# Optimization experiments

Hardware: AMD Instinct MI355X
Metric: run time of the kernel (lower is better)

Reference implementation:

```python
import jax, jax.numpy as jnp
import numpy as np

N_PANO, N_FP = 50000, 10000
D_IN, D_FP, HID, OUT = 128, 64, 128, 64
E_PP, E_PF = 800000, 50000


def _gat(x_src, x_dst, src, dst, Ws, Wd, a_s, a_d, b, n_dst):
    # PyG GATConv (heads=1, add_self_loops=False, bipartite lin_src/lin_dst)
    hs = x_src @ Ws                      # [Ns, C]
    hd = x_dst @ Wd                      # [Nd, C]
    es = hs @ a_s                        # [Ns]
    ed = hd @ a_d                        # [Nd]
    e = jax.nn.leaky_relu(es[src] + ed[dst], negative_slope=0.2)  # [E]
    m = jax.ops.segment_max(e, dst, num_segments=n_dst)
    ex = jnp.exp(e - m[dst])
    den = jax.ops.segment_sum(ex, dst, num_segments=n_dst)
    alpha = ex / den[dst]                # segment softmax over incoming edges
    out = jax.ops.segment_sum(hs[src] * alpha[:, None], dst, num_segments=n_dst)
    return out + b


def setup_inputs() -> dict:
    key = jax.random.key(0)
    ks = jax.random.split(key, 32)
    s_in = 1.0 / np.sqrt(D_IN)
    s_hid = 1.0 / np.sqrt(HID)
    s_fp = 1.0 / np.sqrt(D_FP)
    inp = {
        "x_pano": jax.random.normal(ks[0], (N_PANO, D_IN), jnp.float32),
        "x_fp": jax.random.normal(ks[1], (N_FP, D_FP), jnp.float32),
        # layer 0 (in = D_IN)
        "Ws0": jax.random.normal(ks[2], (D_IN, HID)) * s_in,
        "Wd0": jax.random.normal(ks[3], (D_IN, HID)) * s_in,
        "as0": jax.random.normal(ks[4], (HID,)) * 0.1,
        "ad0": jax.random.normal(ks[5], (HID,)) * 0.1,
        "b0": jnp.zeros((HID,), jnp.float32),
        "Lw0": jax.random.normal(ks[6], (D_IN, HID)) * s_in,
        "Lb0": jnp.zeros((HID,), jnp.float32),
        # layer 1 (in = HID)
        "Ws1": jax.random.normal(ks[7], (HID, HID)) * s_hid,
        "Wd1": jax.random.normal(ks[8], (HID, HID)) * s_hid,
        "as1": jax.random.normal(ks[9], (HID,)) * 0.1,
        "ad1": jax.random.normal(ks[10], (HID,)) * 0.1,
        "b1": jnp.zeros((HID,), jnp.float32),
        "Lw1": jax.random.normal(ks[11], (HID, HID)) * s_hid,
        "Lb1": jnp.zeros((HID,), jnp.float32),
        # translate conv pano -> footprint
        "Wts": jax.random.normal(ks[12], (HID, OUT)) * s_hid,
        "Wtd": jax.random.normal(ks[13], (D_FP, OUT)) * s_fp,
        "ats": jax.random.normal(ks[14], (OUT,)) * 0.1,
        "atd": jax.random.normal(ks[15], (OUT,)) * 0.1,
        "bt": jnp.zeros((OUT,), jnp.float32),
        "edge_pp": jax.random.randint(ks[16], (2, E_PP), 0, N_PANO),
        "edge_pf_src": jax.random.randint(ks[17], (E_PF,), 0, N_PANO),
        "edge_pf_dst": jax.random.randint(ks[18], (E_PF,), 0, N_FP),
    }
    return inp


def reference(x_pano, x_fp, Ws0, Wd0, as0, ad0, b0, Lw0, Lb0,
              Ws1, Wd1, as1, ad1, b1, Lw1, Lb1,
              Wts, Wtd, ats, atd, bt,
              edge_pp, edge_pf_src, edge_pf_dst):
    src, dst = edge_pp[0], edge_pp[1]
    layer_params = [(Ws0, Wd0, as0, ad0, b0, Lw0, Lb0),
                    (Ws1, Wd1, as1, ad1, b1, Lw1, Lb1)]
    h = x_pano
    for (Ws, Wd, a_s, a_d, b, Lw, Lb) in layer_params:
        conv = _gat(h, h, src, dst, Ws, Wd, a_s, a_d, b, N_PANO)
        h = jax.nn.relu(conv + h @ Lw + Lb)
    # HeteroConv with single relation + aggr='sum' == the bipartite conv output
    out_fp = _gat(h, x_fp, edge_pf_src, edge_pf_dst, Wts, Wtd, ats, atd, bt, N_FP)
    return out_fp
```

## Files before the change

kernel.cpp:

```cpp
#include <hip/hip_runtime.h>
#include <hip/hip_bf16.h>
#include <math.h>

#define N_PANO 50000
#define N_FP   10000
#define N_UNI  60000
#define HID    128
#define OUT_C  64
#define E_PP   800000
#define E_PF   50000
#define E_UNI  850000
#define NBKT   235
#define EPB    4096
#define NT_CNT 208

typedef unsigned short ushort_t;
typedef unsigned int uint_t;
typedef __attribute__((ext_vector_type(8))) short short8;
typedef __attribute__((ext_vector_type(4))) float f32x4;

static inline int cdiv(int a, int b) { return (a + b - 1) / b; }

__device__ inline ushort_t f2bf(float x) {
    __hip_bfloat16 h = __float2bfloat16(x);
    return *reinterpret_cast<ushort_t*>(&h);
}
__device__ inline float bfu2f(ushort_t u) {
    return __uint_as_float(((uint_t)u) << 16);
}
__device__ inline float bflo(uint_t u) { return __uint_as_float((u & 0xffffu) << 16); }
__device__ inline float bfhi(uint_t u) { return __uint_as_float(u & 0xffff0000u); }
__device__ inline f32x4 mfma16(short8 a, short8 b, f32x4 c) {
    return __builtin_amdgcn_mfma_f32_16x16x32_bf16(a, b, c, 0, 0, 0);
}

__global__ __launch_bounds__(256) void csr_count_prep(
        const int* __restrict__ pp_dst, const int* __restrict__ pf_dst,
        int* __restrict__ pcnt,
        const float* __restrict__ Ws0, const float* __restrict__ Lw0,
        const float* __restrict__ Ws1, const float* __restrict__ Lw1,
        const float* __restrict__ Wts,
        const float* __restrict__ Wd0, const float* __restrict__ ad0,
        const float* __restrict__ Wd1, const float* __restrict__ ad1,
        const float* __restrict__ Wtd, const float* __restrict__ atd,
        ushort_t* s0, ushort_t* l0, ushort_t* s1, ushort_t* l1, ushort_t* ts,
        float* wed0, float* wed1, float* wedt) {
    __shared__ int hist[NBKT];
    const int tile = blockIdx.x, tid = threadIdx.x;
    if (tile < NT_CNT) {
        for (int t = tid; t < NBKT; t += 256) hist[t] = 0;
        __syncthreads();
        const int e0 = tile * EPB;
        #pragma unroll
        for (int u = 0; u < 16; ++u) {
            int e = e0 + u * 256 + tid;
            int d = -1;
            if (e < E_PP) d = pp_dst[e];
            else if (e < E_UNI) d = N_PANO + pf_dst[e - E_PP];
            if (d >= 0) atomicAdd(&hist[d >> 8], 1);
        }
        __syncthreads();
        for (int t = tid; t < NBKT; t += 256) pcnt[t * NT_CNT + tile] = hist[t];
    } else if (tile < NT_CNT + 288) {
        int i = (tile - NT_CNT) * 256 + tid;
        const float* W; ushort_t* oh;
        int d, NIc, Cc;
        if (i < 65536) {
            int m = i >> 14; d = i & 16383;
            W = (m == 0) ? Ws0 : (m == 1) ? Lw0 : (m == 2) ? Ws1 : Lw1;
            oh = (m == 0) ? s0 : (m == 1) ? l0 : (m == 2) ? s1 : l1;
            NIc = 8; Cc = 128;
        } else if (i < 73728) {
            d = i - 65536; W = Wts; oh = ts;
            NIc = 4; Cc = 64;
        } else return;
        int j = d & 7, l = (d >> 3) & 63;
        int kcl = (d >> 9) & 1;
        int ni = (d >> 10) & (NIc - 1);
        int p = d >> (10 + (NIc == 8 ? 3 : 2));
        int kc = p * 2 + kcl;
        int n = ni * 16 + (l & 15);
        int k = kc * 32 + (l >> 4) * 8 + j;
        oh[d] = f2bf(W[k * Cc + n]);
    } else {
        int r = (tile - NT_CNT - 288) * 4 + (tid >> 6);
        int lane = tid & 63;
        const float* W; const float* a; float* o; int rr, C;
        if (r < 128)      { W = Wd0; a = ad0; o = wed0; rr = r;       C = 128; }
        else if (r < 256) { W = Wd1; a = ad1; o = wed1; rr = r - 128; C = 128; }
        else if (r < 320) { W = Wtd; a = atd; o = wedt; rr = r - 256; C = 64;  }
        else return;
        float s = 0.f;
        for (int j = lane; j < C; j += 64) s += W[rr * C + j] * a[j];
        #pragma unroll
        for (int off = 32; off; off >>= 1) s += __shfl_down(s, off, 64);
        if (lane == 0) o[rr] = s;
    }
}

__global__ __launch_bounds__(256) void csr_scan(const int* __restrict__ pcnt,
                                                int* __restrict__ pexc, int* __restrict__ btot) {
    __shared__ int wsum[4];
    const int b = blockIdx.x, tid = threadIdx.x, lane = tid & 63, wv = tid >> 6;
    int v = (tid < NT_CNT) ? pcnt[b * NT_CNT + tid] : 0;
    int incl = v;
    #pragma unroll
    for (int off = 1; off < 64; off <<= 1) {
        int t = __shfl_up(incl, off, 64);
        if (lane >= off) incl += t;
    }
    if (lane == 63) wsum[wv] = incl;
    __syncthreads();
    if (tid == 0) {
        int run = 0;
        #pragma unroll
        for (int w = 0; w < 4; ++w) { int t = wsum[w]; wsum[w] = run; run += t; }
    }
    __syncthreads();
    int excl = wsum[wv] + incl - v;
    if (tid < NT_CNT) pexc[b * NT_CNT + tid] = excl;
    if (tid == 255) btot[b] = excl;
}

__global__ __launch_bounds__(256) void csr_scatter(const int* __restrict__ pp_src,
                                                   const int* __restrict__ pp_dst,
                                                   const int* __restrict__ pf_src,
                                                   const int* __restrict__ pf_dst,
                                                   const int* __restrict__ pexc,
                                                   const int* __restrict__ btot,
                                                   int* __restrict__ bbase_out,
                                                   int2* __restrict__ tmp) {
    __shared__ int base2[NBKT];
    __shared__ int cur[NBKT];
    __shared__ int wsum[4];
    const int tile = blockIdx.x, tid = threadIdx.x, lane = tid & 63, wv = tid >> 6;
    int v = (tid < NBKT) ? btot[tid] : 0;
    int incl = v;
    #pragma unroll
    for (int off = 1; off < 64; off <<= 1) {
        int t = __shfl_up(incl, off, 64);
        if (lane >= off) incl += t;
    }
    if (lane == 63) wsum[wv] = incl;
    __syncthreads();
    if (tid == 0) {
        int run = 0;
        #pragma unroll
        for (int w = 0; w < 4; ++w) { int t = wsum[w]; wsum[w] = run; run += t; }
    }
    __syncthreads();
    int excl = wsum[wv] + incl - v;
    if (tid < NBKT) {
        base2[tid] = excl + pexc[tid * NT_CNT + tile];
        cur[tid] = 0;
        if (tile == 0) bbase_out[tid] = excl;
    }
    if (tile == 0 && tid == 0) bbase_out[NBKT] = E_UNI;
    __syncthreads();
    const int e0 = tile * EPB;
    #pragma unroll
    for (int u = 0; u < 16; ++u) {
        int e = e0 + u * 256 + tid;
        int d = -1, s = 0;
        if (e < E_PP)       { d = pp_dst[e];                 s = pp_src[e]; }
        else if (e < E_UNI) { d = N_PANO + pf_dst[e - E_PP]; s = pf_src[e - E_PP]; }
        if (d >= 0) {
            int b = d >> 8;
            int p = base2[b] + atomicAdd(&cur[b], 1);
            tmp[p] = make_int2(s, d);
        }
    }
}

__global__ __launch_bounds__(256) void csr_sort(const int2* __restrict__ tmp,
                                                const int* __restrict__ bbase,
                                                int* __restrict__ ptr, int* __restrict__ col) {
    __shared__ int hist[256];
    __shared__ int wsum[4];
    const int b = blockIdx.x, tid = threadIdx.x, lane = tid & 63, wv = tid >> 6;
    const int B0 = bbase[b], B1 = bbase[b + 1];
    hist[tid] = 0;
    __syncthreads();
    for (int e = B0 + tid; e < B1; e += 256) atomicAdd(&hist[tmp[e].y & 255], 1);
    __syncthreads();
    int v = hist[tid];
    int incl = v;
    #pragma unroll
    for (int off = 1; off < 64; off <<= 1) {
        int t = __shfl_up(incl, off, 64);
        if (lane >= off) incl += t;
    }
    if (lane == 63) wsum[wv] = incl;
    __syncthreads();
    if (tid == 0) {
        int run = 0;
        #pragma unroll
        for (int w = 0; w < 4; ++w) { int t = wsum[w]; wsum[w] = run; run += t; }
    }
    __syncthreads();
    int excl = wsum[wv] + incl - v;
    int dg = b * 256 + tid;
    if (dg < N_UNI) ptr[dg] = B0 + excl;
    if (b == NBKT - 1 && tid == 0) ptr[N_UNI] = E_UNI;
    hist[tid] = excl;
    __syncthreads();
    for (int e = B0 + tid; e < B1; e += 256) {
        int2 ed2 = tmp[e];
        int p = B0 + atomicAdd(&hist[ed2.y & 255], 1);
        col[p] = ed2.x;
    }
}

template <int CN, bool DUAL, bool FP32IN>
__global__ __launch_bounds__(256, 2) void gemm_mfma(const float* __restrict__ Xf,
                                                 const ushort_t* __restrict__ Xh,
                                                 const ushort_t* __restrict__ W1, const ushort_t* __restrict__ W2,
                                                 ushort_t* __restrict__ Y1, ushort_t* __restrict__ Y2,
                                                 const float* __restrict__ avec, float* __restrict__ evec,
                                                 const float* __restrict__ wed, float* __restrict__ edv,
                                                 int N) {
    constexpr int NI = CN / 16;
    constexpr int NMAT = DUAL ? 2 : 1;
    constexpr int SLAB = NI * 1024;
    __shared__ ushort_t Bsh[NMAT * SLAB];
    const int tid = threadIdx.x;
    const int w = tid >> 6, l = tid & 63;
    const int col = l & 15, q = l >> 4;
    const int row0 = blockIdx.x * 128 + w * 32;
    f32x4 acc1[2][NI];
    f32x4 acc2[2][DUAL ? NI : 1];
    #pragma unroll
    for (int m = 0; m < 2; ++m)
        #pragma unroll
        for (int ni = 0; ni < NI; ++ni)
            #pragma unroll
            for (int r = 0; r < 4; ++r) acc1[m][ni][r] = 0.f;
    if (DUAL) {
        #pragma unroll
        for (int m = 0; m < 2; ++m)
            #pragma unroll
            for (int ni = 0; ni < NI; ++ni)
                #pragma unroll
                for (int r = 0; r < 4; ++r) acc2[m][ni][r] = 0.f;
    }
    float ped[2] = {0.f, 0.f};

    #pragma unroll
    for (int p = 0; p < 2; ++p) {
        if (p) __syncthreads();
        {
            const uint4* src1 = (const uint4*)W1 + p * (SLAB / 8);
            uint4* dst1 = (uint4*)&Bsh[0];
            #pragma unroll
            for (int f = tid; f < SLAB / 8; f += 256) dst1[f] = src1[f];
            if (DUAL) {
                const uint4* src2 = (const uint4*)W2 + p * (SLAB / 8);
                uint4* dst2 = (uint4*)&Bsh[SLAB];
                #pragma unroll
                for (int f = tid; f < SLAB / 8; f += 256) dst2[f] = src2[f];
            }
        }
        __syncthreads();
        #pragma unroll
        for (int kcl = 0; kcl < 2; ++kcl) {
            const int kc = p * 2 + kcl;
            const int k0 = kc * 32 + q * 8;
            short8 Ah[2];
            #pragma unroll
            for (int m = 0; m < 2; ++m) {
                const int arow = row0 + m * 16 + col;
                if (FP32IN) {
                    float xv[8];
                    if (arow < N) {
                        float4 a0 = *(const float4*)&Xf[(size_t)arow * 128 + k0];
                        float4 a1 = *(const float4*)&Xf[(size_t)arow * 128 + k0 + 4];
                        xv[0] = a0.x; xv[1] = a0.y; xv[2] = a0.z; xv[3] = a0.w;
                        xv[4] = a1.x; xv[5] = a1.y; xv[6] = a1.z; xv[7] = a1.w;
                    } else {
                        #pragma unroll
                        for (int j = 0; j < 8; ++j) xv[j] = 0.f;
                    }
                    #pragma unroll
                    for (int j = 0; j < 8; ++j) Ah[m][j] = (short)f2bf(xv[j]);
                    if (wed) {
                        float4 w0 = *(const float4*)&wed[k0];
                        float4 w1 = *(const float4*)&wed[k0 + 4];
                        ped[m] += xv[0] * w0.x + xv[1] * w0.y + xv[2] * w0.z + xv[3] * w0.w
                                + xv[4] * w1.x + xv[5] * w1.y + xv[6] * w1.z + xv[7] * w1.w;
                    }
                } else {
                    if (arow < N) {
                        Ah[m] = *(const short8*)&Xh[(size_t)arow * 128 + k0];
                    } else {
                        #pragma unroll
                        for (int j = 0; j < 8; ++j) Ah[m][j] = 0;
                    }
                    if (wed) {
                        float4 w0 = *(const float4*)&wed[k0];
                        float4 w1 = *(const float4*)&wed[k0 + 4];
                        float wv[8] = {w0.x, w0.y, w0.z, w0.w, w1.x, w1.y, w1.z, w1.w};
                        #pragma unroll
                        for (int j = 0; j < 8; ++j)
                            ped[m] += bfu2f((ushort_t)Ah[m][j]) * wv[j];
                    }
                }
            }
            #pragma unroll
            for (int ni = 0; ni < NI; ++ni) {
                const int lb = ((ni * 2 + kcl) * 64 + l) * 8;
                short8 B1 = *(const short8*)&Bsh[lb];
                #pragma unroll
                for (int m = 0; m < 2; ++m) acc1[m][ni] = mfma16(Ah[m], B1, acc1[m][ni]);
                if (DUAL) {
                    short8 B2 = *(const short8*)&Bsh[SLAB + lb];
                    #pragma unroll
                    for (int m = 0; m < 2; ++m) acc2[m][ni] = mfma16(Ah[m], B2, acc2[m][ni]);
                }
            }
        }
    }

    #pragma unroll
    for (int m = 0; m < 2; ++m) {
        #pragma unroll
        for (int ni = 0; ni < NI; ++ni) {
            #pragma unroll
            for (int r = 0; r < 4; ++r) {
                int mrow = row0 + m * 16 + q * 4 + r;
                if (mrow < N) {
                    Y1[(size_t)mrow * CN + ni * 16 + col] = f2bf(acc1[m][ni][r]);
                    if (DUAL) Y2[(size_t)mrow * CN + ni * 16 + col] = f2bf(acc2[m][ni][r]);
                }
            }
        }
    }
    float av[NI];
    #pragma unroll
    for (int ni = 0; ni < NI; ++ni) av[ni] = avec[ni * 16 + col];
    #pragma unroll
    for (int m = 0; m < 2; ++m) {
        #pragma unroll
        for (int r = 0; r < 4; ++r) {
            float pp = 0.f;
            #pragma unroll
            for (int ni = 0; ni < NI; ++ni) pp += acc1[m][ni][r] * av[ni];
            pp += __shfl_xor(pp, 1, 64);
            pp += __shfl_xor(pp, 2, 64);
            pp += __shfl_xor(pp, 4, 64);
            pp += __shfl_xor(pp, 8, 64);
            int mrow = row0 + m * 16 + q * 4 + r;
            if (col == 0 && mrow < N) evec[mrow] = pp;
        }
    }
    if (wed) {
        #pragma unroll
        for (int m = 0; m < 2; ++m) {
            ped[m] += __shfl_xor(ped[m], 16, 64);
            ped[m] += __shfl_xor(ped[m], 32, 64);
            int arow = row0 + m * 16 + col;
            if (q == 0 && arow < N) edv[arow] = ped[m];
        }
    }
}

__global__ __launch_bounds__(256) void agg_pano7(const int* __restrict__ ptr, const int* __restrict__ col,
                                                 const float* __restrict__ es, const float* __restrict__ ed,
                                                 const ushort_t* __restrict__ hsb, const ushort_t* __restrict__ linb,
                                                 const float* __restrict__ b, const float* __restrict__ Lb,
                                                 uint_t* __restrict__ hh, int N) {
    int lane = threadIdx.x & 63, wid = threadIdx.x >> 6;
    int nodeA = blockIdx.x * 8 + wid * 2;
    if (nodeA >= N) return;
    int nodeB = nodeA + 1;
    bool hasB = nodeB < N;
    int begA = ptr[nodeA], endA = ptr[nodeA + 1];
    int endB = hasB ? ptr[nodeB + 1] : endA;
    int begB = endA;
    float ednA = ed[nodeA];
    float ednB = hasB ? ed[nodeB] : 0.f;
    const int half = lane >> 5, hl = lane & 31;
    float aA0 = 0.f, aA1 = 0.f, aA2 = 0.f, aA3 = 0.f, dA = 0.f;
    float aB0 = 0.f, aB1 = 0.f, aB2 = 0.f, aB3 = 0.f, dB = 0.f;
    int baseA = begA, baseB = begB;
    while (baseA < endA || baseB < endB) {
        int mA = endA - baseA; mA = mA < 0 ? 0 : (mA > 64 ? 64 : mA);
        int mB = endB - baseB; mB = mB < 0 ? 0 : (mB > 64 ? 64 : mB);
        int sA = 0, sB = 0;
        float wA = 0.f, wB = 0.f;
        if (lane < mA) {
            sA = col[baseA + lane];
            float e = es[sA] + ednA;
            e = fmaxf(e, 0.2f * e);
            wA = __expf(e);
        }
        if (lane < mB) {
            sB = col[baseB + lane];
            float e = es[sB] + ednB;
            e = fmaxf(e, 0.2f * e);
            wB = __expf(e);
        }
        dA += wA; dB += wB;
        {
            int mp = (mA + 1) & ~1;
            int t = 0;
            for (; t + 8 <= mp; t += 8) {
                int i0 = t + half, i1 = t + 2 + half, i2 = t + 4 + half, i3 = t + 6 + half;
                int s0 = __shfl(sA, i0, 64), s1 = __shfl(sA, i1, 64);
                int s2 = __shfl(sA, i2, 64), s3 = __shfl(sA, i3, 64);
                float w0 = __shfl(wA, i0, 64), w1 = __shfl(wA, i1, 64);
                float w2 = __shfl(wA, i2, 64), w3 = __shfl(wA, i3, 64);
                uint2 h0 = *(const uint2*)&hsb[(size_t)s0 * 128 + hl * 4];
                uint2 h1 = *(const uint2*)&hsb[(size_t)s1 * 128 + hl * 4];
                uint2 h2 = *(const uint2*)&hsb[(size_t)s2 * 128 + hl * 4];
                uint2 h3 = *(const uint2*)&hsb[(size_t)s3 * 128 + hl * 4];
                aA0 += w0 * bflo(h0.x) + w1 * bflo(h1.x) + w2 * bflo(h2.x) + w3 * bflo(h3.x);
                aA1 += w0 * bfhi(h0.x) + w1 * bfhi(h1.x) + w2 * bfhi(h2.x) + w3 * bfhi(h3.x);
                aA2 += w0 * bflo(h0.y) + w1 * bflo(h1.y) + w2 * bflo(h2.y) + w3 * bflo(h3.y);
                aA3 += w0 * bfhi(h0.y) + w1 * bfhi(h1.y) + w2 * bfhi(h2.y) + w3 * bfhi(h3.y);
            }
            for (; t < mp; t += 2) {
                int i0 = t + half;
                int s0 = __shfl(sA, i0, 64);
                float w0 = __shfl(wA, i0, 64);
                uint2 h0 = *(const uint2*)&hsb[(size_t)s0 * 128 + hl * 4];
                aA0 += w0 * bflo(h0.x);
                aA1 += w0 * bfhi(h0.x);
                aA2 += w0 * bflo(h0.y);
                aA3 += w0 * bfhi(h0.y);
            }
        }
        {
            int mp = (mB + 1) & ~1;
            int t = 0;
            for (; t + 8 <= mp; t += 8) {
                int i0 = t + half, i1 = t + 2 + half, i2 = t + 4 + half, i3 = t + 6 + half;
                int s0 = __shfl(sB, i0, 64), s1 = __shfl(sB, i1, 64);
                int s2 = __shfl(sB, i2, 64), s3 = __shfl(sB, i3, 64);
                float w0 = __shfl(wB, i0, 64), w1 = __shfl(wB, i1, 64);
                float w2 = __shfl(wB, i2, 64), w3 = __shfl(wB, i3, 64);
                uint2 h0 = *(const uint2*)&hsb[(size_t)s0 * 128 + hl * 4];
                uint2 h1 = *(const uint2*)&hsb[(size_t)s1 * 128 + hl * 4];
                uint2 h2 = *(const uint2*)&hsb[(size_t)s2 * 128 + hl * 4];
                uint2 h3 = *(const uint2*)&hsb[(size_t)s3 * 128 + hl * 4];
                aB0 += w0 * bflo(h0.x) + w1 * bflo(h1.x) + w2 * bflo(h2.x) + w3 * bflo(h3.x);
                aB1 += w0 * bfhi(h0.x) + w1 * bfhi(h1.x) + w2 * bfhi(h2.x) + w3 * bfhi(h3.x);
                aB2 += w0 * bflo(h0.y) + w1 * bflo(h1.y) + w2 * bflo(h2.y) + w3 * bflo(h3.y);
                aB3 += w0 * bfhi(h0.y) + w1 * bfhi(h1.y) + w2 * bfhi(h2.y) + w3 * bfhi(h3.y);
            }
            for (; t < mp; t += 2) {
                int i0 = t + half;
                int s0 = __shfl(sB, i0, 64);
                float w0 = __shfl(wB, i0, 64);
                uint2 h0 = *(const uint2*)&hsb[(size_t)s0 * 128 + hl * 4];
                aB0 += w0 * bflo(h0.x);
                aB1 += w0 * bfhi(h0.x);
                aB2 += w0 * bflo(h0.y);
                aB3 += w0 * bfhi(h0.y);
            }
        }
        baseA += 64; baseB += 64;
    }
    aA0 += __shfl_xor(aA0, 32, 64); aA1 += __shfl_xor(aA1, 32, 64);
    aA2 += __shfl_xor(aA2, 32, 64); aA3 += __shfl_xor(aA3, 32, 64);
    aB0 += __shfl_xor(aB0, 32, 64); aB1 += __shfl_xor(aB1, 32, 64);
    aB2 += __shfl_xor(aB2, 32, 64); aB3 += __shfl_xor(aB3, 32, 64);
    #pragma unroll
    for (int off = 1; off < 64; off <<= 1) dA += __shfl_xor(dA, off, 64);
    #pragma unroll
    for (int off = 1; off < 64; off <<= 1) dB += __shfl_xor(dB, off, 64);
    float invA = (endA > begA) ? (1.f / dA) : 0.f;
    float invB = (endB > begB) ? (1.f / dB) : 0.f;
    int node = half ? nodeB : nodeA;
    if (half == 0 || hasB) {
        float v0 = half ? aB0 : aA0, v1 = half ? aB1 : aA1;
        float v2 = half ? aB2 : aA2, v3 = half ? aB3 : aA3;
        float inv = half ? invB : invA;
        uint2 lv = *(const uint2*)&linb[(size_t)node * 128 + hl * 4];
        float4 bb = *(const float4*)&b[hl * 4];
        float4 lb4 = *(const float4*)&Lb[hl * 4];
        float o0 = fmaxf(v0 * inv + bb.x + bflo(lv.x) + lb4.x, 0.f);
        float o1 = fmaxf(v1 * inv + bb.y + bfhi(lv.x) + lb4.y, 0.f);
        float o2 = fmaxf(v2 * inv + bb.z + bflo(lv.y) + lb4.z, 0.f);
        float o3 = fmaxf(v3 * inv + bb.w + bfhi(lv.y) + lb4.w, 0.f);
        uint2 ov;
        ov.x = (uint_t)f2bf(o0) | ((uint_t)f2bf(o1) << 16);
        ov.y = (uint_t)f2bf(o2) | ((uint_t)f2bf(o3) << 16);
        *(uint2*)&hh[(size_t)node * 64 + hl * 2] = ov;
    }
}

__global__ __launch_bounds__(256) void agg_fp5(const int* __restrict__ ptr, const int* __restrict__ col,
                                               const float* __restrict__ es, const float* __restrict__ x_fp,
                                               const float* __restrict__ wedt,
                                               const ushort_t* __restrict__ hsb, const float* __restrict__ bt,
                                               float* __restrict__ out, int N) {
    int lane = threadIdx.x & 63, wid = threadIdx.x >> 6;
    int node = blockIdx.x * 4 + wid;
    if (node >= N) return;
    int beg = ptr[node], end = ptr[node + 1];
    float edn = x_fp[(size_t)node * 64 + lane] * wedt[lane];
    #pragma unroll
    for (int off = 1; off < 64; off <<= 1) edn += __shfl_xor(edn, off, 64);
    float acc = 0.f, denp = 0.f;
    for (int base = beg; base < end; base += 64) {
        int m = min(64, end - base);
        int s = 0;
        float wgt = 0.f;
        if (lane < m) {
            s = col[base + lane];
            float e = es[s] + edn;
            e = fmaxf(e, 0.2f * e);
            wgt = __expf(e);
        }
        denp += wgt;
        int u = 0;
        for (; u + 4 <= m; u += 4) {
            int s0 = __shfl(s, u, 64), s1 = __shfl(s, u + 1, 64);
            int s2 = __shfl(s, u + 2, 64), s3 = __shfl(s, u + 3, 64);
            float w0 = __shfl(wgt, u, 64), w1 = __shfl(wgt, u + 1, 64);
            float w2 = __shfl(wgt, u + 2, 64), w3 = __shfl(wgt, u + 3, 64);
            float h0 = bfu2f(hsb[(size_t)s0 * 64 + lane]);
            float h1 = bfu2f(hsb[(size_t)s1 * 64 + lane]);
            float h2 = bfu2f(hsb[(size_t)s2 * 64 + lane]);
            float h3 = bfu2f(hsb[(size_t)s3 * 64 + lane]);
            acc += w0 * h0 + w1 * h1 + w2 * h2 + w3 * h3;
        }
        for (; u < m; ++u) {
            int su = __shfl(s, u, 64);
            float wu = __shfl(wgt, u, 64);
            acc += wu * bfu2f(hsb[(size_t)su * 64 + lane]);
        }
    }
    float den = denp;
    #pragma unroll
    for (int off = 1; off < 64; off <<= 1) den += __shfl_xor(den, off, 64);
    float inv = (end > beg) ? (1.f / den) : 0.f;
    out[(size_t)node * 64 + lane] = acc * inv + bt[lane];
}

extern "C" void kernel_launch(void* const* d_in, const int* in_sizes, int n_in,
                              void* d_out, int out_size, void* d_ws, size_t ws_size,
                              hipStream_t stream) {
    const float* x_pano = (const float*)d_in[0];
    const float* x_fp   = (const float*)d_in[1];
    const float* Ws0 = (const float*)d_in[2];
    const float* Wd0 = (const float*)d_in[3];
    const float* as0 = (const float*)d_in[4];
    const float* ad0 = (const float*)d_in[5];
    const float* b0  = (const float*)d_in[6];
    const float* Lw0 = (const float*)d_in[7];
    const float* Lb0 = (const float*)d_in[8];
    const float* Ws1 = (const float*)d_in[9];
    const float* Wd1 = (const float*)d_in[10];
    const float* as1 = (const float*)d_in[11];
    const float* ad1 = (const float*)d_in[12];
    const float* b1  = (const float*)d_in[13];
    const float* Lw1 = (const float*)d_in[14];
    const float* Lb1 = (const float*)d_in[15];
    const float* Wts = (const float*)d_in[16];
    const float* Wtd = (const float*)d_in[17];
    const float* ats = (const float*)d_in[18];
    const float* atd = (const float*)d_in[19];
    const float* bt  = (const float*)d_in[20];
    const int* pp_src = (const int*)d_in[21];
    const int* pp_dst = (const int*)d_in[21] + E_PP;
    const int* pf_src = (const int*)d_in[22];
    const int* pf_dst = (const int*)d_in[23];
    float* out = (float*)d_out;

    char* wsp = (char*)d_ws;
    size_t off = 0;
    auto alloc = [&](size_t bytes) -> char* {
        char* p = wsp + off;
        off += (bytes + 255) & ~(size_t)255;
        return p;
    };
    ushort_t* hsb  = (ushort_t*)alloc(sizeof(ushort_t) * N_PANO * HID);
    ushort_t* linb = (ushort_t*)alloc(sizeof(ushort_t) * N_PANO * HID);
    uint_t* hh     = (uint_t*)alloc(sizeof(uint_t) * N_PANO * 64);
    ushort_t* hstb = (ushort_t*)alloc(sizeof(ushort_t) * N_PANO * OUT_C);
    int2* tmp_e    = (int2*)alloc(sizeof(int2) * E_UNI);
    float* es   = (float*)alloc(sizeof(float) * N_PANO);
    float* ed   = (float*)alloc(sizeof(float) * N_PANO);
    float* wed0 = (float*)alloc(sizeof(float) * HID);
    float* wed1 = (float*)alloc(sizeof(float) * HID);
    float* wedt = (float*)alloc(sizeof(float) * OUT_C);
    ushort_t* s0 = (ushort_t*)alloc(sizeof(ushort_t) * 128 * 128);
    ushort_t* l0 = (ushort_t*)alloc(sizeof(ushort_t) * 128 * 128);
    ushort_t* s1 = (ushort_t*)alloc(sizeof(ushort_t) * 128 * 128);
    ushort_t* l1 = (ushort_t*)alloc(sizeof(ushort_t) * 128 * 128);
    ushort_t* ts = (ushort_t*)alloc(sizeof(ushort_t) * 64 * 128);
    int* pcnt  = (int*)alloc(sizeof(int) * NBKT * NT_CNT);
    int* pexc  = (int*)alloc(sizeof(int) * NBKT * NT_CNT);
    int* btot  = (int*)alloc(sizeof(int) * NBKT);
    int* bbase = (int*)alloc(sizeof(int) * (NBKT + 1));
    int* P     = (int*)alloc(sizeof(int) * (N_UNI + 1));
    int* col_u = (int*)alloc(sizeof(int) * E_UNI);

    csr_count_prep<<<NT_CNT + 288 + 80, 256, 0, stream>>>(
        pp_dst, pf_dst, pcnt, Ws0, Lw0, Ws1, Lw1, Wts,
        Wd0, ad0, Wd1, ad1, Wtd, atd, s0, l0, s1, l1, ts, wed0, wed1, wedt);
    csr_scan<<<NBKT, 256, 0, stream>>>(pcnt, pexc, btot);
    csr_scatter<<<NT_CNT, 256, 0, stream>>>(pp_src, pp_dst, pf_src, pf_dst, pexc, btot, bbase, tmp_e);
    csr_sort<<<NBKT, 256, 0, stream>>>(tmp_e, bbase, P, col_u);

    const int gemm_grid = cdiv(N_PANO, 128);

    gemm_mfma<128, true, true><<<gemm_grid, 256, 0, stream>>>(
        x_pano, nullptr, s0, l0, hsb, linb, as0, es, wed0, ed, N_PANO);
    agg_pano7<<<cdiv(N_PANO, 8), 256, 0, stream>>>(P, col_u, es, ed, hsb, linb, b0, Lb0, hh, N_PANO);

    gemm_mfma<128, true, false><<<gemm_grid, 256, 0, stream>>>(
        nullptr, (const ushort_t*)hh, s1, l1, hsb, linb, as1, es, wed1, ed, N_PANO);
    agg_pano7<<<cdiv(N_PANO, 8), 256, 0, stream>>>(P, col_u, es, ed, hsb, linb, b1, Lb1, hh, N_PANO);

    gemm_mfma<64, false, false><<<gemm_grid, 256, 0, stream>>>(
        nullptr, (const ushort_t*)hh, ts, nullptr, hstb, nullptr, ats, es, nullptr, nullptr, N_PANO);
    agg_fp5<<<cdiv(N_FP, 4), 256, 0, stream>>>(P + N_PANO, col_u, es, x_fp, wedt, hstb, bt, out, N_FP);
}
```

Baseline: 267.4 us.

## Fuse CSR scan into scatter and co-launch scatter with first GEMM

Removes the separate csr_scan kernel: each scatter block recomputes its bucket prefix from the per-tile counts directly. The scatter blocks and the layer-0 GEMM blocks then run in one launch with block-index dispatch, so the independent edge scatter overlaps with the dense projection. This saves two kernel launches and fills idle CUs. In exchange, every scatter block does redundant 208-element row sums per bucket, and shared memory is sized for the larger role.

```diff
diff --git a/kernel.cpp b/kernel.cpp
--- a/kernel.cpp
+++ b/kernel.cpp
@@ -13,6 +13,7 @@
 #define NBKT   235
 #define EPB    4096
 #define NT_CNT 208
+#define NT_GEMM 391
 
 typedef unsigned short ushort_t;
 typedef unsigned int uint_t;
@@ -98,135 +99,20 @@
     }
 }
 
-__global__ __launch_bounds__(256) void csr_scan(const int* __restrict__ pcnt,
-                                                int* __restrict__ pexc, int* __restrict__ btot) {
-    __shared__ int wsum[4];
-    const int b = blockIdx.x, tid = threadIdx.x, lane = tid & 63, wv = tid >> 6;
-    int v = (tid < NT_CNT) ? pcnt[b * NT_CNT + tid] : 0;
-    int incl = v;
-    #pragma unroll
-    for (int off = 1; off < 64; off <<= 1) {
-        int t = __shfl_up(incl, off, 64);
-        if (lane >= off) incl += t;
-    }
-    if (lane == 63) wsum[wv] = incl;
-    __syncthreads();
-    if (tid == 0) {
-        int run = 0;
-        #pragma unroll
-        for (int w = 0; w < 4; ++w) { int t = wsum[w]; wsum[w] = run; run += t; }
-    }
-    __syncthreads();
-    int excl = wsum[wv] + incl - v;
-    if (tid < NT_CNT) pexc[b * NT_CNT + tid] = excl;
-    if (tid == 255) btot[b] = excl;
-}
-
-__global__ __launch_bounds__(256) void csr_scatter(const int* __restrict__ pp_src,
-                                                   const int* __restrict__ pp_dst,
-                                                   const int* __restrict__ pf_src,
-                                                   const int* __restrict__ pf_dst,
-                                                   const int* __restrict__ pexc,
-                                                   const int* __restrict__ btot,
-                                                   int* __restrict__ bbase_out,
-                                                   int2* __restrict__ tmp) {
-    __shared__ int base2[NBKT];
-    __shared__ int cur[NBKT];
-    __shared__ int wsum[4];
-    const int tile = blockIdx.x, tid = threadIdx.x, lane = tid & 63, wv = tid >> 6;
-    int v = (tid < NBKT) ? btot[tid] : 0;
-    int incl = v;
-    #pragma unroll
-    for (int off = 1; off < 64; off <<= 1) {
-        int t = __shfl_up(incl, off, 64);
-        if (lane >= off) incl += t;
-    }
-    if (lane == 63) wsum[wv] = incl;
-    __syncthreads();
-    if (tid == 0) {
-        int run = 0;
-        #pragma unroll
-        for (int w = 0; w < 4; ++w) { int t = wsum[w]; wsum[w] = run; run += t; }
-    }
-    __syncthreads();
-    int excl = wsum[wv] + incl - v;
-    if (tid < NBKT) {
-        base2[tid] = excl + pexc[tid * NT_CNT + tile];
-        cur[tid] = 0;
-        if (tile == 0) bbase_out[tid] = excl;
-    }
-    if (tile == 0 && tid == 0) bbase_out[NBKT] = E_UNI;
-    __syncthreads();
-    const int e0 = tile * EPB;
-    #pragma unroll
-    for (int u = 0; u < 16; ++u) {
-        int e = e0 + u * 256 + tid;
-        int d = -1, s = 0;
-        if (e < E_PP)       { d = pp_dst[e];                 s = pp_src[e]; }
-        else if (e < E_UNI) { d = N_PANO + pf_dst[e - E_PP]; s = pf_src[e - E_PP]; }
-        if (d >= 0) {
-            int b = d >> 8;
-            int p = base2[b] + atomicAdd(&cur[b], 1);
-            tmp[p] = make_int2(s, d);
-        }
-    }
-}
-
-__global__ __launch_bounds__(256) void csr_sort(const int2* __restrict__ tmp,
-                                                const int* __restrict__ bbase,
-                                                int* __restrict__ ptr, int* __restrict__ col) {
-    __shared__ int hist[256];
-    __shared__ int wsum[4];
-    const int b = blockIdx.x, tid = threadIdx.x, lane = tid & 63, wv = tid >> 6;
-    const int B0 = bbase[b], B1 = bbase[b + 1];
-    hist[tid] = 0;
-    __syncthreads();
-    for (int e = B0 + tid; e < B1; e += 256) atomicAdd(&hist[tmp[e].y & 255], 1);
-    __syncthreads();
-    int v = hist[tid];
-    int incl = v;
-    #pragma unroll
-    for (int off = 1; off < 64; off <<= 1) {
-        int t = __shfl_up(incl, off, 64);
-        if (lane >= off) incl += t;
-    }
-    if (lane == 63) wsum[wv] = incl;
-    __syncthreads();
-    if (tid == 0) {
-        int run = 0;
-        #pragma unroll
-        for (int w = 0; w < 4; ++w) { int t = wsum[w]; wsum[w] = run; run += t; }
-    }
-    __syncthreads();
-    int excl = wsum[wv] + incl - v;
-    int dg = b * 256 + tid;
-    if (dg < N_UNI) ptr[dg] = B0 + excl;
-    if (b == NBKT - 1 && tid == 0) ptr[N_UNI] = E_UNI;
-    hist[tid] = excl;
-    __syncthreads();
-    for (int e = B0 + tid; e < B1; e += 256) {
-        int2 ed2 = tmp[e];
-        int p = B0 + atomicAdd(&hist[ed2.y & 255], 1);
-        col[p] = ed2.x;
-    }
-}
-
 template <int CN, bool DUAL, bool FP32IN>
-__global__ __launch_bounds__(256, 2) void gemm_mfma(const float* __restrict__ Xf,
-                                                 const ushort_t* __restrict__ Xh,
-                                                 const ushort_t* __restrict__ W1, const ushort_t* __restrict__ W2,
-                                                 ushort_t* __restrict__ Y1, ushort_t* __restrict__ Y2,
-                                                 const float* __restrict__ avec, float* __restrict__ evec,
-                                                 const float* __restrict__ wed, float* __restrict__ edv,
-                                                 int N) {
+__device__ void gemm_body(int tile, char* smem,
+                          const float* __restrict__ Xf, const ushort_t* __restrict__ Xh,
+                          const ushort_t* __restrict__ W1, const ushort_t* __restrict__ W2,
+                          ushort_t* __restrict__ Y1, ushort_t* __restrict__ Y2,
+                          const float* __restrict__ avec, float* __restrict__ evec,
+                          const float* __restrict__ wed, float* __restrict__ edv, int N) {
     constexpr int NI = CN / 16;
-    constexpr int NMAT = DUAL ? 2 : 1;
     constexpr int SLAB = NI * 1024;
-    __shared__ ushort_t Bsh[NMAT * SLAB];
+    ushort_t* Bsh = (ushort_t*)smem;
     const int tid = threadIdx.x;
     const int w = tid >> 6, l = tid & 63;
     const int col = l & 15, q = l >> 4;
-    const int row0 = blockIdx.x * 128 + w * 32;
+    const int row0 = tile * 128 + w * 32;
     f32x4 acc1[2][NI];
     f32x4 acc2[2][DUAL ? NI : 1];
     #pragma unroll
@@ -363,6 +249,130 @@
     }
 }
 
+__device__ void scatter_body(int tile, char* smem,
+                             const int* __restrict__ pp_src, const int* __restrict__ pp_dst,
+                             const int* __restrict__ pf_src, const int* __restrict__ pf_dst,
+                             const int* __restrict__ pcnt, int* __restrict__ bbase_out,
+                             int2* __restrict__ tmp) {
+    int* base2 = (int*)smem;
+    int* cur   = base2 + NBKT;
+    int* wsum  = cur + NBKT;
+    const int tid = threadIdx.x, lane = tid & 63, wv = tid >> 6;
+    int rowsum = 0, myprefix = 0;
+    if (tid < NBKT) {
+        const int* row = pcnt + tid * NT_CNT;
+        for (int t = 0; t < NT_CNT; ++t) {
+            int c = row[t];
+            rowsum += c;
+            if (t < tile) myprefix += c;
+        }
+    }
+    int v = (tid < NBKT) ? rowsum : 0;
+    int incl = v;
+    #pragma unroll
+    for (int off = 1; off < 64; off <<= 1) {
+        int t = __shfl_up(incl, off, 64);
+        if (lane >= off) incl += t;
+    }
+    if (lane == 63) wsum[wv] = incl;
+    __syncthreads();
+    if (tid == 0) {
+        int run = 0;
+        #pragma unroll
+        for (int w = 0; w < 4; ++w) { int t = wsum[w]; wsum[w] = run; run += t; }
+    }
+    __syncthreads();
+    int bexcl = wsum[wv] + incl - v;
+    if (tid < NBKT) {
+        base2[tid] = bexcl + myprefix;
+        cur[tid] = 0;
+        if (tile == 0) bbase_out[tid] = bexcl;
+    }
+    if (tile == 0 && tid == 0) bbase_out[NBKT] = E_UNI;
+    __syncthreads();
+    const int e0 = tile * EPB;
+    #pragma unroll
+    for (int u = 0; u < 16; ++u) {
+        int e = e0 + u * 256 + tid;
+        int d = -1, s = 0;
+        if (e < E_PP)       { d = pp_dst[e];                 s = pp_src[e]; }
+        else if (e < E_UNI) { d = N_PANO + pf_dst[e - E_PP]; s = pf_src[e - E_PP]; }
+        if (d >= 0) {
+            int b = d >> 8;
+            int p = base2[b] + atomicAdd(&cur[b], 1);
+            tmp[p] = make_int2(s, d);
+        }
+    }
+}
+
+__global__ __launch_bounds__(256, 2) void scatter_gemm0(
+        const int* __restrict__ pp_src, const int* __restrict__ pp_dst,
+        const int* __restrict__ pf_src, const int* __restrict__ pf_dst,
+        const int* __restrict__ pcnt, int* __restrict__ bbase_out, int2* __restrict__ tmp,
+        const float* __restrict__ x_pano,
+        const ushort_t* __restrict__ s0, const ushort_t* __restrict__ l0,
+        ushort_t* __restrict__ hsb, ushort_t* __restrict__ linb,
+        const float* __restrict__ as0, float* __restrict__ es,
+        const float* __restrict__ wed0, float* __restrict__ ed) {
+    __shared__ __align__(16) char smem[32768];
+    if (blockIdx.x < NT_CNT)
+        scatter_body(blockIdx.x, smem, pp_src, pp_dst, pf_src, pf_dst, pcnt, bbase_out, tmp);
+    else
+        gemm_body<128, true, true>(blockIdx.x - NT_CNT, smem, x_pano, nullptr, s0, l0,
+                                   hsb, linb, as0, es, wed0, ed, N_PANO);
+}
+
+template <int CN, bool DUAL, bool FP32IN>
+__global__ __launch_bounds__(256, 2) void gemm_mfma(const float* __restrict__ Xf,
+                                                 const ushort_t* __restrict__ Xh,
+                                                 const ushort_t* __restrict__ W1, const ushort_t* __restrict__ W2,
+                                                 ushort_t* __restrict__ Y1, ushort_t* __restrict__ Y2,
+                                                 const float* __restrict__ avec, float* __restrict__ evec,
+                                                 const float* __restrict__ wed, float* __restrict__ edv,
+                                                 int N) {
+    __shared__ __align__(16) char smem[(DUAL ? 2 : 1) * (CN / 16) * 2048];
+    gemm_body<CN, DUAL, FP32IN>(blockIdx.x, smem, Xf, Xh, W1, W2, Y1, Y2, avec, evec, wed, edv, N);
+}
+
+__global__ __launch_bounds__(256) void csr_sort(const int2* __restrict__ tmp,
+                                                const int* __restrict__ bbase,
+                                                int* __restrict__ ptr, int* __restrict__ col) {
+    __shared__ int hist[256];
+    __shared__ int wsum[4];
+    const int b = blockIdx.x, tid = threadIdx.x, lane = tid & 63, wv = tid >> 6;
+    const int B0 = bbase[b], B1 = bbase[b + 1];
+    hist[tid] = 0;
+    __syncthreads();
+    for (int e = B0 + tid; e < B1; e += 256) atomicAdd(&hist[tmp[e].y & 255], 1);
+    __syncthreads();
+    int v = hist[tid];
+    int incl = v;
+    #pragma unroll
+    for (int off = 1; off < 64; off <<= 1) {
+        int t = __shfl_up(incl, off, 64);
+        if (lane >= off) incl += t;
+    }
+    if (lane == 63) wsum[wv] = incl;
+    __syncthreads();
+    if (tid == 0) {
+        int run = 0;
+        #pragma unroll
+        for (int w = 0; w < 4; ++w) { int t = wsum[w]; wsum[w] = run; run += t; }
+    }
+    __syncthreads();
+    int excl = wsum[wv] + incl - v;
+    int dg = b * 256 + tid;
+    if (dg < N_UNI) ptr[dg] = B0 + excl;
+    if (b == NBKT - 1 && tid == 0) ptr[N_UNI] = E_UNI;
+    hist[tid] = excl;
+    __syncthreads();
+    for (int e = B0 + tid; e < B1; e += 256) {
+        int2 ed2 = tmp[e];
+        int p = B0 + atomicAdd(&hist[ed2.y & 255], 1);
+        col[p] = ed2.x;
+    }
+}
+
 __global__ __launch_bounds__(256) void agg_pano7(const int* __restrict__ ptr, const int* __restrict__ col,
                                                  const float* __restrict__ es, const float* __restrict__ ed,
                                                  const ushort_t* __restrict__ hsb, const ushort_t* __restrict__ linb,
@@ -591,8 +601,6 @@
     ushort_t* l1 = (ushort_t*)alloc(sizeof(ushort_t) * 128 * 128);
     ushort_t* ts = (ushort_t*)alloc(sizeof(ushort_t) * 64 * 128);
     int* pcnt  = (int*)alloc(sizeof(int) * NBKT * NT_CNT);
-    int* pexc  = (int*)alloc(sizeof(int) * NBKT * NT_CNT);
-    int* btot  = (int*)alloc(sizeof(int) * NBKT);
     int* bbase = (int*)alloc(sizeof(int) * (NBKT + 1));
     int* P     = (int*)alloc(sizeof(int) * (N_UNI + 1));
     int* col_u = (int*)alloc(sizeof(int) * E_UNI);
@@ -600,21 +608,22 @@
     csr_count_prep<<<NT_CNT + 288 + 80, 256, 0, stream>>>(
         pp_dst, pf_dst, pcnt, Ws0, Lw0, Ws1, Lw1, Wts,
         Wd0, ad0, Wd1, ad1, Wtd, atd, s0, l0, s1, l1, ts, wed0, wed1, wedt);
-    csr_scan<<<NBKT, 256, 0, stream>>>(pcnt, pexc, btot);
-    csr_scatter<<<NT_CNT, 256, 0, stream>>>(pp_src, pp_dst, pf_src, pf_dst, pexc, btot, bbase, tmp_e);
+
+    scatter_gemm0<<<NT_CNT + NT_GEMM, 256, 0, stream>>>(
+        pp_src, pp_dst, pf_src, pf_dst, pcnt, bbase, tmp_e,
+        x_pano, s0, l0, hsb, linb, as0, es, wed0, ed);
+
     csr_sort<<<NBKT, 256, 0, stream>>>(tmp_e, bbase, P, col_u);
 
-    const int gemm_grid = cdiv(N_PANO, 128);
-
-    gemm_mfma<128, true, true><<<gemm_grid, 256, 0, stream>>>(
-        x_pano, nullptr, s0, l0, hsb, linb, as0, es, wed0, ed, N_PANO);
     agg_pano7<<<cdiv(N_PANO, 8), 256, 0, stream>>>(P, col_u, es, ed, hsb, linb, b0, Lb0, hh, N_PANO);
 
-    gemm_mfma<128, true, false><<<gemm_grid, 256, 0, stream>>>(
+    gemm_mfma<128, true, false><<<NT_GEMM, 256, 0, stream>>>(
         nullptr, (const ushort_t*)hh, s1, l1, hsb, linb, as1, es, wed1, ed, N_PANO);
+
     agg_pano7<<<cdiv(N_PANO, 8), 256, 0, stream>>>(P, col_u, es, ed, hsb, linb, b1, Lb1, hh, N_PANO);
 
-    gemm_mfma<64, false, false><<<gemm_grid, 256, 0, stream>>>(
+    gemm_mfma<64, false, false><<<NT_GEMM, 256, 0, stream>>>(
         nullptr, (const ushort_t*)hh, ts, nullptr, hstb, nullptr, ats, es, nullptr, nullptr, N_PANO);
+
     agg_fp5<<<cdiv(N_FP, 4), 256, 0, stream>>>(P + N_PANO, col_u, es, x_fp, wedt, hstb, bt, out, N_FP);
 }
```

Result: no change. 266.1 us (-0.5%).
